# Performance work log

Hardware: AMD Instinct MI355X
Metric: run time of the kernel (lower is better)

Reference implementation:

```python
import jax, jax.numpy as jnp
import numpy as np

NQ, BS, HW, D, H, DFF = 300, 16, 2048, 256, 8, 2048
HD2 = (2 * D) // H   # cross-attn head dim (query/key), 64
VHD = D // H         # value head dim, 32
EPS = 1e-5


def _lin_params(key, din, dout):
    kw, kb = jax.random.split(key)
    w = jax.random.normal(kw, (din, dout), jnp.float32) * 0.02
    b = jax.random.normal(kb, (dout,), jnp.float32) * 0.02
    return w, b


def setup_inputs() -> dict:
    key = jax.random.key(0)
    ks = jax.random.split(key, 24)
    inp = {
        'tgt': jax.random.normal(ks[0], (NQ, BS, D), jnp.float32),
        'memory': jax.random.normal(ks[1], (HW, BS, D), jnp.float32),
        'pos': jax.random.normal(ks[2], (HW, BS, D), jnp.float32),
        'cls_query_pos': jax.random.normal(ks[3], (NQ, BS, D), jnp.float32),
        'cls_query_sine_embed': jax.random.normal(ks[4], (NQ, BS, D), jnp.float32),
    }
    names = [('w_qc', 'b_qc', D, D), ('w_qp', 'b_qp', D, D), ('w_kc', 'b_kc', D, D),
             ('w_kp', 'b_kp', D, D), ('w_v', 'b_v', D, D), ('w_qs', 'b_qs', D, D),
             ('wq', 'bq', 2 * D, 2 * D), ('wk', 'bk', 2 * D, 2 * D),
             ('wv', 'bv', D, D), ('wo', 'bo', D, D),
             ('w1', 'b1', D, DFF), ('w2', 'b2', DFF, D)]
    for i, (wn, bn, din, dout) in enumerate(names):
        w, b = _lin_params(ks[5 + i], din, dout)
        inp[wn], inp[bn] = w, b
    inp['g2'] = jnp.ones((D,), jnp.float32)
    inp['be2'] = jnp.zeros((D,), jnp.float32)
    inp['g3'] = jnp.ones((D,), jnp.float32)
    inp['be3'] = jnp.zeros((D,), jnp.float32)
    return inp


def _ln(x, g, b):
    m = x.mean(-1, keepdims=True)
    v = ((x - m) ** 2).mean(-1, keepdims=True)
    return (x - m) * jax.lax.rsqrt(v + EPS) * g + b


def reference(tgt, memory, pos, cls_query_pos, cls_query_sine_embed,
              w_qc, b_qc, w_qp, b_qp, w_kc, b_kc, w_kp, b_kp, w_v, b_v,
              w_qs, b_qs, wq, bq, wk, bk, wv, bv, wo, bo,
              w1, b1, w2, b2, g2, be2, g3, be3):
    nq, bs, d = tgt.shape
    hw = memory.shape[0]
    # conditional cross-attention projections (is_first=True path)
    q_content = tgt @ w_qc + b_qc
    k_content = memory @ w_kc + b_kc
    v_in = memory @ w_v + b_v
    k_pos = pos @ w_kp + b_kp
    q_pos = cls_query_pos @ w_qp + b_qp
    q = (q_content + q_pos).reshape(nq, bs, H, d // H)
    sine = (cls_query_sine_embed @ w_qs + b_qs).reshape(nq, bs, H, d // H)
    q = jnp.concatenate([q, sine], axis=3).reshape(nq, bs, 2 * d)
    k = (k_content + k_pos).reshape(hw, bs, H, d // H)
    kp = k_pos.reshape(hw, bs, H, d // H)
    k = jnp.concatenate([k, kp], axis=3).reshape(hw, bs, 2 * d)
    # MultiheadAttention(embed_dim=2d, nhead, vdim=d): internal q/k/v/out projs
    scale = 1.0 / jnp.sqrt(jnp.float32(HD2))
    qh = ((q @ wq + bq) * scale).reshape(nq, bs, H, HD2)
    kh = (k @ wk + bk).reshape(hw, bs, H, HD2)
    vh = (v_in @ wv + bv).reshape(hw, bs, H, VHD)
    logits = jnp.einsum('qbhd,kbhd->bhqk', qh, kh)
    attn = jax.nn.softmax(logits, axis=-1)              # [bs, H, nq, hw]
    ctx = jnp.einsum('bhqk,kbhd->qbhd', attn, vh).reshape(nq, bs, d)
    tgt2 = ctx @ wo + bo
    attn_avg = attn.mean(axis=1)                        # averaged over heads
    # residual + norm + FFN + norm (dropout disabled / eval)
    x = _ln(tgt + tgt2, g2, be2)
    ffn = jax.nn.relu(x @ w1 + b1) @ w2 + b2
    x = _ln(x + ffn, g3, be3)
    return (x, attn_avg)
```

## Files before the change

kernel.cpp:

```cpp
#include <hip/hip_runtime.h>

typedef unsigned short u16;
typedef __attribute__((ext_vector_type(8))) short short8;
typedef __attribute__((ext_vector_type(4))) float f32x4;

#define MFMA16(a, b, c) __builtin_amdgcn_mfma_f32_16x16x32_bf16(a, b, c, 0, 0, 0)

__device__ __forceinline__ float bf2f(u16 u) {
    return __uint_as_float(((unsigned)u) << 16);
}
__device__ __forceinline__ u16 f2bf(float f) {
    unsigned u = __float_as_uint(f);
    u += 0x7fff + ((u >> 16) & 1);
    return (u16)(u >> 16);
}

__global__ __launch_bounds__(256) void cvt2(const float* __restrict__ a,
                                            const float* __restrict__ b,
                                            u16* __restrict__ A, u16* __restrict__ B) {
    size_t i = ((size_t)blockIdx.x * 256 + threadIdx.x) * 4;
    float4 va = *(const float4*)(a + i);
    float4 vb = *(const float4*)(b + i);
    u16 ta[4] = {f2bf(va.x), f2bf(va.y), f2bf(va.z), f2bf(va.w)};
    u16 tb[4] = {f2bf(vb.x), f2bf(vb.y), f2bf(vb.z), f2bf(vb.w)};
    *(uint2*)(A + i) = *(uint2*)ta;
    *(uint2*)(B + i) = *(uint2*)tb;
}


__global__ __launch_bounds__(256) void fold_q(const float* __restrict__ w_qc,
                                              const float* __restrict__ w_qp,
                                              const float* __restrict__ w_qs,
                                              const float* __restrict__ wq,
                                              u16* __restrict__ WQ3T) {
    int o = blockIdx.x * 256 + threadIdx.x;
    int k0 = blockIdx.y * 4;
    int seg = k0 >> 8, kb = k0 & 255;
    const float* wsrc = (seg == 0) ? w_qc : ((seg == 1) ? w_qp : w_qs);
    int sOff = (seg == 2) ? 32 : 0;
    const float* wcol = wq + o;
    float acc[4] = {0.f, 0.f, 0.f, 0.f};
#pragma unroll 8
    for (int c = 0; c < 256; c++) {
        int mc = (c >> 5) * 64 + (c & 31) + sOff;
        float w0 = wcol[(size_t)mc * 512];
#pragma unroll
        for (int j = 0; j < 4; j++)
            acc[j] += wsrc[(size_t)(kb + j) * 256 + c] * w0;
    }
    u16 outv[4];
#pragma unroll
    for (int j = 0; j < 4; j++) outv[j] = f2bf(acc[j] * 0.125f);
    *(uint2*)(WQ3T + (size_t)o * 768 + k0) = *(uint2*)outv;
}

__global__ __launch_bounds__(256) void fold_k(const float* __restrict__ w_kc,
                                              const float* __restrict__ w_kp,
                                              const float* __restrict__ wk,
                                              u16* __restrict__ WK2T) {
    int o = blockIdx.x * 256 + threadIdx.x;
    int k0 = blockIdx.y * 4;
    bool second = k0 >= 256;
    int kb = second ? k0 - 256 : k0;
    const float* wcol = wk + o;
    float acc[4] = {0.f, 0.f, 0.f, 0.f};
    if (second) {
#pragma unroll 8
        for (int c = 0; c < 256; c++) {
            int mc = (c >> 5) * 64 + (c & 31);
            float w0 = wcol[(size_t)mc * 512] + wcol[(size_t)(mc + 32) * 512];
#pragma unroll
            for (int j = 0; j < 4; j++)
                acc[j] += w_kp[(size_t)(kb + j) * 256 + c] * w0;
        }
    } else {
#pragma unroll 8
        for (int c = 0; c < 256; c++) {
            int mc = (c >> 5) * 64 + (c & 31);
            float w0 = wcol[(size_t)mc * 512];
#pragma unroll
            for (int j = 0; j < 4; j++)
                acc[j] += w_kc[(size_t)(kb + j) * 256 + c] * w0;
        }
    }
    u16 outv[4];
#pragma unroll
    for (int j = 0; j < 4; j++) outv[j] = f2bf(acc[j]);
    *(uint2*)(WK2T + (size_t)o * 512 + k0) = *(uint2*)outv;
}

__global__ __launch_bounds__(256) void fold_v(const float* __restrict__ w_v,
                                              const float* __restrict__ wv_w,
                                              u16* __restrict__ WV2T) {
    int o = threadIdx.x;
    int k0 = blockIdx.y * 4;
    float acc[4] = {0.f, 0.f, 0.f, 0.f};
#pragma unroll 8
    for (int c = 0; c < 256; c++) {
        float w0 = wv_w[(size_t)c * 256 + o];
#pragma unroll
        for (int j = 0; j < 4; j++)
            acc[j] += w_v[(size_t)(k0 + j) * 256 + c] * w0;
    }
    u16 outv[4];
#pragma unroll
    for (int j = 0; j < 4; j++) outv[j] = f2bf(acc[j]);
    *(uint2*)(WV2T + (size_t)o * 256 + k0) = *(uint2*)outv;
}

__global__ __launch_bounds__(256) void fold_bias(
    const float* b_qc, const float* b_qp, const float* b_qs, const float* wq, const float* bq,
    const float* b_kc, const float* b_kp, const float* wk, const float* bk,
    const float* b_v, const float* wv_w, const float* bv,
    float* BQF, float* BKF, float* BVF) {
    __shared__ float red[4][64];
    int tid = threadIdx.x, lane = tid & 63, wave = tid >> 6;
    int blk = blockIdx.x;
    float acc = 0.f;
    if (blk < 8) {
        int o = blk * 64 + lane;
#pragma unroll 4
        for (int c = wave * 64; c < wave * 64 + 64; c++) {
            int mc = (c >> 5) * 64 + (c & 31);
            acc += (b_qc[c] + b_qp[c]) * wq[(size_t)mc * 512 + o];
            acc += b_qs[c] * wq[(size_t)(mc + 32) * 512 + o];
        }
        red[wave][lane] = acc;
        __syncthreads();
        if (wave == 0)
            BQF[o] = (bq[o] + red[0][lane] + red[1][lane] + red[2][lane] + red[3][lane]) * 0.125f;
    } else if (blk < 16) {
        int o = (blk - 8) * 64 + lane;
#pragma unroll 4
        for (int c = wave * 64; c < wave * 64 + 64; c++) {
            int mc = (c >> 5) * 64 + (c & 31);
            acc += (b_kc[c] + b_kp[c]) * wk[(size_t)mc * 512 + o];
            acc += b_kp[c] * wk[(size_t)(mc + 32) * 512 + o];
        }
        red[wave][lane] = acc;
        __syncthreads();
        if (wave == 0)
            BKF[o] = bk[o] + red[0][lane] + red[1][lane] + red[2][lane] + red[3][lane];
    } else {
        int o = (blk - 16) * 64 + lane;
#pragma unroll 4
        for (int c = wave * 64; c < wave * 64 + 64; c++)
            acc += b_v[c] * wv_w[(size_t)c * 256 + o];
        red[wave][lane] = acc;
        __syncthreads();
        if (wave == 0)
            BVF[o] = bv[o] + red[0][lane] + red[1][lane] + red[2][lane] + red[3][lane];
    }
}

__global__ __launch_bounds__(256) void transpose_f2b(const float* __restrict__ src,
                                                     u16* __restrict__ dst, int R, int C) {
    __shared__ float tile[32][33];
    int c0 = blockIdx.x * 32, r0 = blockIdx.y * 32;
    int t = threadIdx.x;
    int j = t & 31, i0 = (t >> 5) * 4;
#pragma unroll
    for (int ii = 0; ii < 4; ii++)
        tile[i0 + ii][j] = src[(size_t)(r0 + i0 + ii) * C + c0 + j];
    __syncthreads();
    int i2 = t & 31, j0 = (t >> 5) * 4;
#pragma unroll
    for (int jj = 0; jj < 4; jj++)
        dst[(size_t)(c0 + j0 + jj) * R + r0 + i2] = f2bf(tile[i2][j0 + jj]);
}

#define APAD 40
__global__ __launch_bounds__(256) void gemm_bt(
    const void* __restrict__ A0v, const void* __restrict__ A1v, const void* __restrict__ A2v,
    int astride, int a_f32, const u16* __restrict__ BT, const float* __restrict__ bias,
    u16* __restrict__ C, int M, int N, int K, int mode) {
    __shared__ u16 As[128 * APAD];
    __shared__ u16 Bs[128 * APAD];
    int tid = threadIdx.x;
    int wave = tid >> 6, lane = tid & 63;
    int l15 = lane & 15, quad = lane >> 4;
    int wm = (wave >> 1) * 64, wn = (wave & 1) * 64;
    int gm0 = blockIdx.x * 128, gn0 = blockIdx.y * 128;
    f32x4 acc[4][4] = {};
    for (int k0 = 0; k0 < K; k0 += 32) {
        const void* ap;
        int kin;
        if (astride == 256) {
            int p = k0 >> 8;
            ap = (p == 0) ? A0v : ((p == 1) ? A1v : A2v);
            kin = k0 & 255;
        } else {
            ap = A0v;
            kin = k0;
        }
#pragma unroll
        for (int i = 0; i < 2; i++) {
            int idx = tid * 2 + i;
            int row = idx >> 2, seg = (idx & 3) * 8;
            int grow = gm0 + row;
            u16 tmp[8];
            if (a_f32) {
                float vv[8] = {0.f, 0.f, 0.f, 0.f, 0.f, 0.f, 0.f, 0.f};
                if (grow < M) {
                    const float* apf = (const float*)ap;
                    float4 u0 = *(const float4*)(apf + (size_t)grow * astride + kin + seg);
                    float4 u1 = *(const float4*)(apf + (size_t)grow * astride + kin + seg + 4);
                    vv[0] = u0.x; vv[1] = u0.y; vv[2] = u0.z; vv[3] = u0.w;
                    vv[4] = u1.x; vv[5] = u1.y; vv[6] = u1.z; vv[7] = u1.w;
                }
#pragma unroll
                for (int e = 0; e < 8; e++) tmp[e] = f2bf(vv[e]);
            } else {
                uint4 v;
                v.x = v.y = v.z = v.w = 0;
                if (grow < M) v = *(const uint4*)((const u16*)ap + (size_t)grow * astride + kin + seg);
                *(uint4*)tmp = v;
            }
            *(uint4*)(&As[row * APAD + seg]) = *(uint4*)tmp;
            int nrow = gn0 + row;
            uint4 w = *(const uint4*)(BT + (size_t)nrow * K + k0 + seg);
            *(uint4*)(&Bs[row * APAD + seg]) = w;
        }
        __syncthreads();
        short8 afr[4], bfr[4];
#pragma unroll
        for (int i = 0; i < 4; i++)
            afr[i] = *(const short8*)(&As[(wm + i * 16 + l15) * APAD + quad * 8]);
#pragma unroll
        for (int j = 0; j < 4; j++)
            bfr[j] = *(const short8*)(&Bs[(wn + j * 16 + l15) * APAD + quad * 8]);
#pragma unroll
        for (int i = 0; i < 4; i++)
#pragma unroll
            for (int j = 0; j < 4; j++) acc[i][j] = MFMA16(afr[i], bfr[j], acc[i][j]);
        __syncthreads();
    }
#pragma unroll
    for (int i = 0; i < 4; i++) {
        int row = gm0 + wm + i * 16 + quad * 4;
#pragma unroll
        for (int j = 0; j < 4; j++) {
            int col = gn0 + wn + j * 16 + l15;
            float bvv = bias[col];
#pragma unroll
            for (int r = 0; r < 4; r++) {
                int grow = row + r;
                if (grow < M) {
                    float v = acc[i][j][r] + bvv;
                    if (mode == 1) v = fmaxf(v, 0.f);
                    C[(size_t)grow * N + col] = f2bf(v);
                }
            }
        }
    }
}

__global__ __launch_bounds__(256) void attn_a(const u16* __restrict__ qh,
                                              const u16* __restrict__ kh,
                                              const u16* __restrict__ vhr,
                                              u16* __restrict__ ctxbuf,
                                              float* __restrict__ z8inv) {
    int qt = blockIdx.x, h = blockIdx.y, b = blockIdx.z;
    __shared__ u16 Qt[64 * 72];
    __shared__ u16 Kc[128 * 72];
    __shared__ u16 Pt[64 * 136];
    __shared__ u16 VTc[32 * 136];
    int tid = threadIdx.x, wave = tid >> 6, lane = tid & 63;
    int l15 = lane & 15, quad = lane >> 4;
    int q0 = qt * 64;
#pragma unroll
    for (int i = 0; i < 2; i++) {
        int idx = tid * 2 + i;
        int row = idx >> 3, seg = (idx & 7) * 8;
        uint4 v;
        v.x = v.y = v.z = v.w = 0;
        int q = q0 + row;
        if (q < 300) v = *(const uint4*)(qh + ((size_t)q * 16 + b) * 512 + h * 64 + seg);
        *(uint4*)(&Qt[row * 72 + seg]) = v;
    }
    const f32x4 zf = {0.f, 0.f, 0.f, 0.f};
    f32x4 cacc[2] = {};
    float zrow[4] = {0.f, 0.f, 0.f, 0.f};
    for (int kc0 = 0; kc0 < 2048; kc0 += 128) {
#pragma unroll
        for (int i = 0; i < 4; i++) {
            int idx = tid * 4 + i;
            int row = idx >> 3, seg = (idx & 7) * 8;
            *(uint4*)(&Kc[row * 72 + seg]) =
                *(const uint4*)(kh + ((size_t)(kc0 + row) * 16 + b) * 512 + h * 64 + seg);
        }
#pragma unroll
        for (int i = 0; i < 2; i++) {
            int idx = tid * 2 + i;
            int kk = idx >> 2, dseg = (idx & 3) * 8;
            u16 tmp[8];
            *(uint4*)tmp = *(const uint4*)(vhr + ((size_t)(kc0 + kk) * 16 + b) * 256 + h * 32 + dseg);
#pragma unroll
            for (int e = 0; e < 8; e++) VTc[(dseg + e) * 136 + kk] = tmp[e];
        }
        __syncthreads();
        f32x4 sacc[8];
#pragma unroll
        for (int t = 0; t < 8; t++) sacc[t] = zf;
#pragma unroll
        for (int d0 = 0; d0 < 64; d0 += 32) {
            short8 af = *(const short8*)(&Qt[(wave * 16 + l15) * 72 + d0 + quad * 8]);
#pragma unroll
            for (int t = 0; t < 8; t++) {
                short8 bf = *(const short8*)(&Kc[(t * 16 + l15) * 72 + d0 + quad * 8]);
                sacc[t] = MFMA16(af, bf, sacc[t]);
            }
        }
#pragma unroll
        for (int t = 0; t < 8; t++) {
#pragma unroll
            for (int r = 0; r < 4; r++) {
                float p = __expf(sacc[t][r]);
                zrow[r] += p;
                Pt[(wave * 16 + quad * 4 + r) * 136 + t * 16 + l15] = f2bf(p);
            }
        }
#pragma unroll
        for (int kk0 = 0; kk0 < 128; kk0 += 32) {
            short8 af = *(const short8*)(&Pt[(wave * 16 + l15) * 136 + kk0 + quad * 8]);
#pragma unroll
            for (int t = 0; t < 2; t++) {
                short8 bf = *(const short8*)(&VTc[(t * 16 + l15) * 136 + kk0 + quad * 8]);
                cacc[t] = MFMA16(af, bf, cacc[t]);
            }
        }
        __syncthreads();
    }
#pragma unroll
    for (int r = 0; r < 4; r++) {
        float z = zrow[r];
        z += __shfl_xor(z, 1);
        z += __shfl_xor(z, 2);
        z += __shfl_xor(z, 4);
        z += __shfl_xor(z, 8);
        zrow[r] = z;
    }
#pragma unroll
    for (int r = 0; r < 4; r++) {
        int q = q0 + wave * 16 + quad * 4 + r;
        if (q < 300) {
            float rz = 1.0f / zrow[r];
#pragma unroll
            for (int t = 0; t < 2; t++)
                ctxbuf[((size_t)q * 16 + b) * 256 + h * 32 + t * 16 + l15] = f2bf(cacc[t][r] * rz);
            if (l15 == 0) z8inv[((size_t)b * 8 + h) * 320 + q] = rz * 0.125f;
        }
    }
}

__global__ __launch_bounds__(256) void attn_b(const u16* __restrict__ qh,
                                              const u16* __restrict__ kh,
                                              const float* __restrict__ z8inv,
                                              float* __restrict__ out1) {
    int kc0 = blockIdx.x * 128, qt = blockIdx.y, b = blockIdx.z;
    __shared__ u16 Qt[64 * 72];
    __shared__ u16 Kc[128 * 72];
    int tid = threadIdx.x, wave = tid >> 6, lane = tid & 63;
    int l15 = lane & 15, quad = lane >> 4;
    int q0 = qt * 64;
    const f32x4 zf = {0.f, 0.f, 0.f, 0.f};
    float avg[8][4] = {};
    for (int h = 0; h < 8; h++) {
#pragma unroll
        for (int i = 0; i < 2; i++) {
            int idx = tid * 2 + i;
            int row = idx >> 3, seg = (idx & 7) * 8;
            uint4 v;
            v.x = v.y = v.z = v.w = 0;
            int q = q0 + row;
            if (q < 300) v = *(const uint4*)(qh + ((size_t)q * 16 + b) * 512 + h * 64 + seg);
            *(uint4*)(&Qt[row * 72 + seg]) = v;
        }
#pragma unroll
        for (int i = 0; i < 4; i++) {
            int idx = tid * 4 + i;
            int row = idx >> 3, seg = (idx & 7) * 8;
            *(uint4*)(&Kc[row * 72 + seg]) =
                *(const uint4*)(kh + ((size_t)(kc0 + row) * 16 + b) * 512 + h * 64 + seg);
        }
        __syncthreads();
        f32x4 sacc[8];
#pragma unroll
        for (int t = 0; t < 8; t++) sacc[t] = zf;
#pragma unroll
        for (int d0 = 0; d0 < 64; d0 += 32) {
            short8 af = *(const short8*)(&Qt[(wave * 16 + l15) * 72 + d0 + quad * 8]);
#pragma unroll
            for (int t = 0; t < 8; t++) {
                short8 bf = *(const short8*)(&Kc[(t * 16 + l15) * 72 + d0 + quad * 8]);
                sacc[t] = MFMA16(af, bf, sacc[t]);
            }
        }
        float zi[4];
#pragma unroll
        for (int r = 0; r < 4; r++) {
            int q = q0 + wave * 16 + quad * 4 + r;
            zi[r] = z8inv[((size_t)b * 8 + h) * 320 + (q < 319 ? q : 319)];
        }
#pragma unroll
        for (int t = 0; t < 8; t++)
#pragma unroll
            for (int r = 0; r < 4; r++) avg[t][r] += __expf(sacc[t][r]) * zi[r];
        __syncthreads();
    }
#pragma unroll
    for (int r = 0; r < 4; r++) {
        int q = q0 + wave * 16 + quad * 4 + r;
        if (q < 300) {
#pragma unroll
            for (int t = 0; t < 8; t++)
                out1[((size_t)b * 300 + q) * 2048 + kc0 + t * 16 + l15] = avg[t][r];
        }
    }
}

__global__ __launch_bounds__(256) void ln_kernel(const void* __restrict__ a, int a_f32,
                                                 const u16* __restrict__ bres,
                                                 const float* __restrict__ g,
                                                 const float* __restrict__ be,
                                                 void* __restrict__ out, int out_f32) {
    int row = blockIdx.x, t = threadIdx.x;
    float av = a_f32 ? ((const float*)a)[(size_t)row * 256 + t]
                     : bf2f(((const u16*)a)[(size_t)row * 256 + t]);
    float v = av + bf2f(bres[(size_t)row * 256 + t]);
    float s = v, sq = v * v;
#pragma unroll
    for (int o = 32; o; o >>= 1) {
        s += __shfl_xor(s, o);
        sq += __shfl_xor(sq, o);
    }
    __shared__ float red[8];
    int wave = t >> 6, lane = t & 63;
    if (lane == 0) {
        red[wave] = s;
        red[4 + wave] = sq;
    }
    __syncthreads();
    s = red[0] + red[1] + red[2] + red[3];
    sq = red[4] + red[5] + red[6] + red[7];
    float mean = s * (1.f / 256.f);
    float var = sq * (1.f / 256.f) - mean * mean;
    float rs = rsqrtf(var + 1e-5f);
    float res = (v - mean) * rs * g[t] + be[t];
    if (out_f32) ((float*)out)[(size_t)row * 256 + t] = res;
    else ((u16*)out)[(size_t)row * 256 + t] = f2bf(res);
}

extern "C" void kernel_launch(void* const* d_in, const int* in_sizes, int n_in,
                              void* d_out, int out_size, void* d_ws, size_t ws_size,
                              hipStream_t stream) {
    (void)in_sizes; (void)n_in; (void)out_size; (void)ws_size;
    const float* tgt = (const float*)d_in[0];
    const float* mem = (const float*)d_in[1];
    const float* pos = (const float*)d_in[2];
    const float* qpos = (const float*)d_in[3];
    const float* qsine = (const float*)d_in[4];
    const float* w_qc = (const float*)d_in[5];
    const float* b_qc = (const float*)d_in[6];
    const float* w_qp = (const float*)d_in[7];
    const float* b_qp = (const float*)d_in[8];
    const float* w_kc = (const float*)d_in[9];
    const float* b_kc = (const float*)d_in[10];
    const float* w_kp = (const float*)d_in[11];
    const float* b_kp = (const float*)d_in[12];
    const float* w_v = (const float*)d_in[13];
    const float* b_v = (const float*)d_in[14];
    const float* w_qs = (const float*)d_in[15];
    const float* b_qs = (const float*)d_in[16];
    const float* wq = (const float*)d_in[17];
    const float* bq = (const float*)d_in[18];
    const float* wk = (const float*)d_in[19];
    const float* bk = (const float*)d_in[20];
    const float* wv_w = (const float*)d_in[21];
    const float* bv = (const float*)d_in[22];
    const float* wo = (const float*)d_in[23];
    const float* bo = (const float*)d_in[24];
    const float* w1 = (const float*)d_in[25];
    const float* b1 = (const float*)d_in[26];
    const float* w2 = (const float*)d_in[27];
    const float* b2 = (const float*)d_in[28];
    const float* g2 = (const float*)d_in[29];
    const float* be2 = (const float*)d_in[30];
    const float* g3 = (const float*)d_in[31];
    const float* be3 = (const float*)d_in[32];

    char* ws = (char*)d_ws;
    u16* WQ3T = (u16*)(ws + 0x000000);
    u16* WK2T = (u16*)(ws + 0x0C0000);
    u16* WV2T = (u16*)(ws + 0x140000);
    u16* WOT  = (u16*)(ws + 0x160000);
    u16* W1T  = (u16*)(ws + 0x180000);
    u16* W2T  = (u16*)(ws + 0x280000);
    float* BQF = (float*)(ws + 0x380000);
    float* BKF = (float*)(ws + 0x381000);
    float* BVF = (float*)(ws + 0x382000);
    float* Z8  = (float*)(ws + 0x390000);
    u16* QH  = (u16*)(ws + 0x400000);
    u16* KH  = (u16*)(ws + 0x900000);
    u16* CTX = (u16*)(ws + 0x2900000);
    u16* TGT2 = (u16*)(ws + 0x900000);
    u16* XBUF = (u16*)(ws + 0xB60000);
    u16* FFNB = (u16*)(ws + 0xDC0000);
    u16* HBUF = (u16*)(ws + 0x1020000);

    float* out0 = (float*)d_out;
    float* out1 = out0 + 1228800;
    u16* MB  = (u16*)out1;
    u16* PB  = MB + 8388608;
    u16* VHR = PB;

    cvt2<<<8192, 256, 0, stream>>>(mem, pos, MB, PB);
    fold_q<<<dim3(2, 192), 256, 0, stream>>>(w_qc, w_qp, w_qs, wq, WQ3T);
    fold_k<<<dim3(2, 128), 256, 0, stream>>>(w_kc, w_kp, wk, WK2T);
    fold_v<<<dim3(1, 64), 256, 0, stream>>>(w_v, wv_w, WV2T);
    fold_bias<<<20, 256, 0, stream>>>(b_qc, b_qp, b_qs, wq, bq, b_kc, b_kp, wk, bk,
                                      b_v, wv_w, bv, BQF, BKF, BVF);
    transpose_f2b<<<dim3(8, 8), 256, 0, stream>>>(wo, WOT, 256, 256);
    transpose_f2b<<<dim3(64, 8), 256, 0, stream>>>(w1, W1T, 256, 2048);
    transpose_f2b<<<dim3(8, 64), 256, 0, stream>>>(w2, W2T, 2048, 256);

    gemm_bt<<<dim3(38, 4), 256, 0, stream>>>(tgt, qpos, qsine, 256, 1, WQ3T, BQF, QH, 4800, 512, 768, 0);
    gemm_bt<<<dim3(256, 4), 256, 0, stream>>>(MB, PB, nullptr, 256, 0, WK2T, BKF, KH, 32768, 512, 512, 0);
    gemm_bt<<<dim3(256, 2), 256, 0, stream>>>(MB, nullptr, nullptr, 256, 0, WV2T, BVF, VHR, 32768, 256, 256, 0);

    attn_a<<<dim3(5, 8, 16), 256, 0, stream>>>(QH, KH, VHR, CTX, Z8);
    attn_b<<<dim3(16, 5, 16), 256, 0, stream>>>(QH, KH, Z8, out1);

    gemm_bt<<<dim3(38, 2), 256, 0, stream>>>(CTX, nullptr, nullptr, 256, 0, WOT, bo, TGT2, 4800, 256, 256, 0);
    ln_kernel<<<4800, 256, 0, stream>>>(tgt, 1, TGT2, g2, be2, XBUF, 0);
    gemm_bt<<<dim3(38, 16), 256, 0, stream>>>(XBUF, nullptr, nullptr, 256, 0, W1T, b1, HBUF, 4800, 2048, 256, 1);
    gemm_bt<<<dim3(38, 2), 256, 0, stream>>>(HBUF, nullptr, nullptr, 2048, 0, W2T, b2, FFNB, 4800, 256, 2048, 0);
    ln_kernel<<<4800, 256, 0, stream>>>(XBUF, 0, FFNB, g3, be3, out0, 1);
}
```

Before: 592.4 us.

## Split attention over key halves with pre-transposed V and separate normalization

The attention-context kernel now splits the 2048 keys into two halves, which doubles the grid to 1280 blocks. Each half writes an unnormalized fp32 context and a partial row sum, and a new attn_norm kernel combines the halves and normalizes. V is transposed once into a per-head layout by a new kernel, so attn_a reads V fragments straight from global memory instead of transposing them through LDS. Q is held in registers and the block index is swizzled to spread (b,h) groups across XCDs. The cost is two extra launches and extra fp32 partial-buffer traffic.

```diff
diff --git a/kernel.cpp b/kernel.cpp
--- a/kernel.cpp
+++ b/kernel.cpp
@@ -255,102 +255,128 @@
     }
 }
 
-__global__ __launch_bounds__(256) void attn_a(const u16* __restrict__ qh,
-                                              const u16* __restrict__ kh,
-                                              const u16* __restrict__ vhr,
-                                              u16* __restrict__ ctxbuf,
-                                              float* __restrict__ z8inv) {
-    int qt = blockIdx.x, h = blockIdx.y, b = blockIdx.z;
-    __shared__ u16 Qt[64 * 72];
-    __shared__ u16 Kc[128 * 72];
-    __shared__ u16 Pt[64 * 136];
-    __shared__ u16 VTc[32 * 136];
+__global__ __launch_bounds__(256) void transpose_v(const u16* __restrict__ vhr,
+                                                   u16* __restrict__ vt) {
+    int k0 = blockIdx.x * 128, b = blockIdx.y, h = blockIdx.z;
+    int tid = threadIdx.x;
+#pragma unroll
+    for (int i = 0; i < 2; i++) {
+        int idx = tid * 2 + i;
+        int d = idx >> 4, ks = (idx & 15) * 8;
+        u16 o[8];
+#pragma unroll
+        for (int e = 0; e < 8; e++)
+            o[e] = vhr[((size_t)(k0 + ks + e) * 16 + b) * 256 + h * 32 + d];
+        *(uint4*)(vt + ((size_t)(b * 8 + h) * 32 + d) * 2048 + k0 + ks) = *(uint4*)o;
+    }
+}
+
+__global__ __launch_bounds__(256, 5) void attn_a(const u16* __restrict__ qh,
+                                                 const u16* __restrict__ kh,
+                                                 const u16* __restrict__ vt,
+                                                 float* __restrict__ ctxp,
+                                                 float* __restrict__ zp) {
+    int l = blockIdx.x;
+    int w = (l & 7) * 160 + (l >> 3);
+    int g = w / 10;
+    int iw = w - g * 10;
+    int kc = iw / 5;
+    int qt = iw - kc * 5;
+    int h = g & 7, b = g >> 3;
+    __shared__ u16 Kc[64 * 72];
+    __shared__ u16 Pt[64 * 72];
     int tid = threadIdx.x, wave = tid >> 6, lane = tid & 63;
     int l15 = lane & 15, quad = lane >> 4;
     int q0 = qt * 64;
-#pragma unroll
-    for (int i = 0; i < 2; i++) {
-        int idx = tid * 2 + i;
-        int row = idx >> 3, seg = (idx & 7) * 8;
-        uint4 v;
-        v.x = v.y = v.z = v.w = 0;
-        int q = q0 + row;
-        if (q < 300) v = *(const uint4*)(qh + ((size_t)q * 16 + b) * 512 + h * 64 + seg);
-        *(uint4*)(&Qt[row * 72 + seg]) = v;
-    }
-    const f32x4 zf = {0.f, 0.f, 0.f, 0.f};
+    int kb0 = kc * 1024;
+    short8 qf[2];
+    {
+        short8 qz = {};
+        qf[0] = qz;
+        qf[1] = qz;
+        int q = q0 + wave * 16 + l15;
+        if (q < 300) {
+            const u16* qp = qh + ((size_t)q * 16 + b) * 512 + h * 64 + quad * 8;
+            qf[0] = *(const short8*)(qp);
+            qf[1] = *(const short8*)(qp + 32);
+        }
+    }
+    const u16* kbase = kh + (size_t)kb0 * 8192 + b * 512 + h * 64;
+    const u16* vbase = vt + ((size_t)(b * 8 + h) * 32) * 2048 + kb0;
     f32x4 cacc[2] = {};
-    float zrow[4] = {0.f, 0.f, 0.f, 0.f};
-    for (int kc0 = 0; kc0 < 2048; kc0 += 128) {
-#pragma unroll
-        for (int i = 0; i < 4; i++) {
-            int idx = tid * 4 + i;
+    float zl = 0.f;
+    for (int it = 0; it < 16; ++it) {
+#pragma unroll
+        for (int i2 = 0; i2 < 2; i2++) {
+            int idx = tid * 2 + i2;
             int row = idx >> 3, seg = (idx & 7) * 8;
             *(uint4*)(&Kc[row * 72 + seg]) =
-                *(const uint4*)(kh + ((size_t)(kc0 + row) * 16 + b) * 512 + h * 64 + seg);
-        }
-#pragma unroll
-        for (int i = 0; i < 2; i++) {
-            int idx = tid * 2 + i;
-            int kk = idx >> 2, dseg = (idx & 3) * 8;
-            u16 tmp[8];
-            *(uint4*)tmp = *(const uint4*)(vhr + ((size_t)(kc0 + kk) * 16 + b) * 256 + h * 32 + dseg);
-#pragma unroll
-            for (int e = 0; e < 8; e++) VTc[(dseg + e) * 136 + kk] = tmp[e];
-        }
-        __syncthreads();
-        f32x4 sacc[8];
-#pragma unroll
-        for (int t = 0; t < 8; t++) sacc[t] = zf;
-#pragma unroll
-        for (int d0 = 0; d0 < 64; d0 += 32) {
-            short8 af = *(const short8*)(&Qt[(wave * 16 + l15) * 72 + d0 + quad * 8]);
-#pragma unroll
-            for (int t = 0; t < 8; t++) {
-                short8 bf = *(const short8*)(&Kc[(t * 16 + l15) * 72 + d0 + quad * 8]);
-                sacc[t] = MFMA16(af, bf, sacc[t]);
+                *(const uint4*)(kbase + (size_t)(it * 64 + row) * 8192 + seg);
+        }
+        __syncthreads();
+        f32x4 sacc[4] = {};
+#pragma unroll
+        for (int d0 = 0; d0 < 2; d0++)
+#pragma unroll
+            for (int t = 0; t < 4; t++) {
+                short8 af = *(const short8*)(&Kc[(t * 16 + l15) * 72 + d0 * 32 + quad * 8]);
+                sacc[t] = MFMA16(af, qf[d0], sacc[t]);
             }
-        }
-#pragma unroll
-        for (int t = 0; t < 8; t++) {
+        __syncthreads();
+#pragma unroll
+        for (int t = 0; t < 4; t++) {
+            u16 pk[4];
 #pragma unroll
             for (int r = 0; r < 4; r++) {
                 float p = __expf(sacc[t][r]);
-                zrow[r] += p;
-                Pt[(wave * 16 + quad * 4 + r) * 136 + t * 16 + l15] = f2bf(p);
+                zl += p;
+                pk[r] = f2bf(p);
             }
-        }
-#pragma unroll
-        for (int kk0 = 0; kk0 < 128; kk0 += 32) {
-            short8 af = *(const short8*)(&Pt[(wave * 16 + l15) * 136 + kk0 + quad * 8]);
+            *(uint2*)(&Pt[(wave * 16 + l15) * 72 + t * 16 + quad * 4]) = *(uint2*)pk;
+        }
+#pragma unroll
+        for (int kk = 0; kk < 2; kk++) {
+            short8 pa = *(const short8*)(&Pt[(wave * 16 + l15) * 72 + kk * 32 + quad * 8]);
 #pragma unroll
             for (int t = 0; t < 2; t++) {
-                short8 bf = *(const short8*)(&VTc[(t * 16 + l15) * 136 + kk0 + quad * 8]);
-                cacc[t] = MFMA16(af, bf, cacc[t]);
+                short8 bf = *(const short8*)(vbase + (size_t)(t * 16 + l15) * 2048 +
+                                             it * 64 + kk * 32 + quad * 8);
+                cacc[t] = MFMA16(pa, bf, cacc[t]);
             }
         }
-        __syncthreads();
-    }
-#pragma unroll
-    for (int r = 0; r < 4; r++) {
-        float z = zrow[r];
-        z += __shfl_xor(z, 1);
-        z += __shfl_xor(z, 2);
-        z += __shfl_xor(z, 4);
-        z += __shfl_xor(z, 8);
-        zrow[r] = z;
-    }
+    }
+    zl += __shfl_xor(zl, 16);
+    zl += __shfl_xor(zl, 32);
+    if (quad == 0) {
+        int q = q0 + wave * 16 + l15;
+        if (q < 300) zp[((size_t)kc * 128 + b * 8 + h) * 320 + q] = zl;
+    }
+    float* cp = ctxp + (size_t)kc * 5120 * 256;
 #pragma unroll
     for (int r = 0; r < 4; r++) {
         int q = q0 + wave * 16 + quad * 4 + r;
         if (q < 300) {
-            float rz = 1.0f / zrow[r];
 #pragma unroll
             for (int t = 0; t < 2; t++)
-                ctxbuf[((size_t)q * 16 + b) * 256 + h * 32 + t * 16 + l15] = f2bf(cacc[t][r] * rz);
-            if (l15 == 0) z8inv[((size_t)b * 8 + h) * 320 + q] = rz * 0.125f;
-        }
-    }
+                cp[((size_t)q * 16 + b) * 256 + h * 32 + t * 16 + l15] = cacc[t][r];
+        }
+    }
+}
+
+__global__ __launch_bounds__(256) void attn_norm(const float* __restrict__ ctxp,
+                                                 const float* __restrict__ zp,
+                                                 u16* __restrict__ ctx,
+                                                 float* __restrict__ z8inv) {
+    int row = blockIdx.x;
+    int t = threadIdx.x;
+    int q = row >> 4, b = row & 15;
+    int h = t >> 5;
+    float c = ctxp[(size_t)row * 256 + t] + ctxp[(size_t)5120 * 256 + (size_t)row * 256 + t];
+    size_t zi = ((size_t)b * 8 + h) * 320 + q;
+    float z = zp[zi] + zp[(size_t)128 * 320 + zi];
+    float rz = 1.0f / z;
+    ctx[(size_t)row * 256 + t] = f2bf(c * rz);
+    if ((t & 31) == 0) z8inv[zi] = rz * 0.125f;
 }
 
 __global__ __launch_bounds__(256) void attn_b(const u16* __restrict__ qh,
@@ -513,6 +539,9 @@
     u16* MB  = (u16*)out1;
     u16* PB  = MB + 8388608;
     u16* VHR = PB;
+    u16* VT  = MB;
+    float* CTXP = (float*)PB;
+    float* ZP   = CTXP + (size_t)2 * 5120 * 256;
 
     cvt2<<<8192, 256, 0, stream>>>(mem, pos, MB, PB);
     fold_q<<<dim3(2, 192), 256, 0, stream>>>(w_qc, w_qp, w_qs, wq, WQ3T);
@@ -528,7 +557,9 @@
     gemm_bt<<<dim3(256, 4), 256, 0, stream>>>(MB, PB, nullptr, 256, 0, WK2T, BKF, KH, 32768, 512, 512, 0);
     gemm_bt<<<dim3(256, 2), 256, 0, stream>>>(MB, nullptr, nullptr, 256, 0, WV2T, BVF, VHR, 32768, 256, 256, 0);
 
-    attn_a<<<dim3(5, 8, 16), 256, 0, stream>>>(QH, KH, VHR, CTX, Z8);
+    transpose_v<<<dim3(16, 16, 8), 256, 0, stream>>>(VHR, VT);
+    attn_a<<<1280, 256, 0, stream>>>(QH, KH, VT, CTXP, ZP);
+    attn_norm<<<4800, 256, 0, stream>>>(CTXP, ZP, CTX, Z8);
     attn_b<<<dim3(16, 5, 16), 256, 0, stream>>>(QH, KH, Z8, out1);
 
     gemm_bt<<<dim3(38, 2), 256, 0, stream>>>(CTX, nullptr, nullptr, 256, 0, WOT, bo, TGT2, 4800, 256, 256, 0);
```

Result: no change. 588.5 us (-0.7%).
